# Performance work log

Measured on AMD Instinct MI355X. Metric: run time of the kernel, lower is better.

The kernel has to match this reference:

```python
import jax, jax.numpy as jnp
import numpy as np

B = 256        # graphs per batch
NPG = 256      # nodes per graph (uniform -> to_dense_batch is a reshape, mask = ones)
NTOT = B * NPG
E = 1_048_576
F_IN = 64
HID = 128
HEADS = 5
K1, K2 = 32, 8
MEMH = 100
NCLS = 12
TAU = 1.0
EPS = 1e-8


def setup_inputs() -> dict:
    key = jax.random.key(0)
    ks = jax.random.split(key, 24)
    f32 = jnp.float32
    def nrm(k, shape, s=0.05):
        return jax.random.normal(k, shape, f32) * s
    inp = {
        "x": jax.random.normal(ks[0], (NTOT, F_IN), f32),
        "edge_index": jax.random.randint(ks[1], (2, E), 0, NTOT, jnp.int32),
        "batch": jnp.repeat(jnp.arange(B, dtype=jnp.int32), NPG),
        # GraphConv q0 (num_feats -> hidden): lin_rel (bias) + lin_root (no bias)
        "W_rel0": nrm(ks[2], (F_IN, HID)), "b_rel0": jnp.zeros((HID,), f32),
        "W_root0": nrm(ks[3], (F_IN, HID)),
        # GraphConv q1 (hidden -> hidden)
        "W_rel1": nrm(ks[4], (HID, HID)), "b_rel1": jnp.zeros((HID,), f32),
        "W_root1": nrm(ks[5], (HID, HID)),
        # BatchNorm1d affine params
        "bn_gamma": jnp.ones((HID,), f32), "bn_beta": jnp.zeros((HID,), f32),
        # MemConv layer 0: keys ~ U[0,1) as torch.rand, conv1x1 [heads], lin F->MEMH
        "keys0": jax.random.uniform(ks[6], (HEADS, K1, HID), f32),
        "convw0": nrm(ks[7], (HEADS,), 0.2),
        "lin_W0": nrm(ks[8], (HID, MEMH)), "lin_b0": jnp.zeros((MEMH,), f32),
        # MemConv layer 1 (num_features = mem_hidden_dim)
        "keys1": jax.random.uniform(ks[9], (HEADS, K2, MEMH), f32),
        "convw1": nrm(ks[10], (HEADS,), 0.2),
        "lin_W1": nrm(ks[11], (MEMH, MEMH)), "lin_b1": jnp.zeros((MEMH,), f32),
        # MLP head
        "mlp_W1": nrm(ks[12], (MEMH, 50)), "mlp_b1": jnp.zeros((50,), f32),
        "mlp_W2": nrm(ks[13], (50, NCLS)), "mlp_b2": jnp.zeros((NCLS,), f32),
    }
    return inp


def _graph_conv(x, src, dst, W_rel, b_rel, W_root):
    # PyG GraphConv, aggr='add': out_i = lin_rel(sum_{j in N(i)} x_j) + lin_root(x_i)
    msg = x[src]                                            # [E, F] gather
    aggr = jax.ops.segment_sum(msg, dst, num_segments=NTOT)  # [N, F] scatter-add
    return aggr @ W_rel + b_rel + x @ W_root


def _kl_reg(C):
    P = C ** 2
    cn = C.sum(axis=-2, keepdims=True) + EPS
    P = P / cn
    pn = P.sum(axis=-1, keepdims=True) + EPS
    P = P / pn
    return 100.0 * (P * (jnp.log(P + EPS) - jnp.log(C + EPS))).sum()


def _mem_conv(Q, keys, conv_w, lin_W, lin_b, mask):
    # Q: [B, N, F]; keys: [H, K, F]; mask: [B, N] or None
    # pairwise L2 distance via norm expansion (same math as the broadcast-diff)
    qsq = (Q * Q).sum(-1)                                   # [B, N]
    ksq = (keys * keys).sum(-1)                             # [H, K]
    qk = jnp.einsum('bnf,hkf->bhnk', Q, keys)               # [B, H, N, K]
    d2 = qsq[:, None, :, None] + ksq[None, :, None, :] - 2.0 * qk
    C = jnp.sqrt(jnp.maximum(d2, 1e-12))
    if mask is not None:
        ext = mask[:, None, :, None]                        # [B,1,N,1]
        C = C * ext
    # gmn kernel: student-t style normalization over keys
    C = (1.0 + C * C / TAU) ** (-(0.5 * TAU + 0.5))
    C = C / C.sum(axis=-1, keepdims=True)
    if mask is not None:
        C = C * ext
    # conv1x1 over heads (no bias) then squeeze head dim
    C = jnp.einsum('h,bhnk->bnk', conv_w, C)
    C = jax.nn.softmax(C, axis=-1)                          # [B, N, K]
    if mask is not None:
        C = C * mask[:, :, None]
    kl = _kl_reg(C)
    V = jnp.einsum('bnk,bnf->bkf', C, Q)                    # [B, K, F]
    out = jax.nn.leaky_relu(V @ lin_W + lin_b)              # slope 0.01 (torch default)
    return out, kl


def reference(x, edge_index, batch, W_rel0, b_rel0, W_root0, W_rel1, b_rel1,
              W_root1, bn_gamma, bn_beta, keys0, convw0, lin_W0, lin_b0,
              keys1, convw1, lin_W1, lin_b1, mlp_W1, mlp_b1, mlp_W2, mlp_b2):
    src, dst = edge_index[0], edge_index[1]
    q = jax.nn.relu(_graph_conv(x, src, dst, W_rel0, b_rel0, W_root0))
    q = jax.nn.relu(_graph_conv(q, src, dst, W_rel1, b_rel1, W_root1))
    # BatchNorm1d over all (padded-)node rows, training stats, eps=1e-5
    mu = q.mean(axis=0)
    var = ((q - mu) ** 2).mean(axis=0)
    q = (q - mu) * jax.lax.rsqrt(var + 1e-5) * bn_gamma + bn_beta
    Q = q.reshape(B, NPG, HID)                              # to_dense_batch (uniform graphs)
    mask = jnp.ones((B, NPG), jnp.float32)
    q1, kl1 = _mem_conv(Q, keys0, convw0, lin_W0, lin_b0, mask)
    q2, kl2 = _mem_conv(q1, keys1, convw1, lin_W1, lin_b1, None)
    h = q2.mean(axis=-2)                                    # [B, MEMH]
    yh = jax.nn.leaky_relu(h @ mlp_W1 + mlp_b1) @ mlp_W2 + mlp_b2
    return yh, (kl1 + kl2) / NTOT
```

## Files before the change

### kernel.cpp

```cpp
#include <hip/hip_runtime.h>
#include <hip/hip_bf16.h>

#define NTOT   65536
#define NEDGE  1048576
#define HEADS  5
#define K1     32
#define K2     8
#define MEMH   100
#define EPSF   1e-8f

#define OFF_DEG     0x0000000
#define OFF_CURSOR  0x0040000
#define OFF_WT1     0x0040000
#define OFF_WT2     0x0050000
#define OFF_OFFS    0x0080000
#define OFF_BNSUM   0x00C0000
#define OFF_BNSQ    0x00C0400
#define OFF_SCALE   0x00C0800
#define OFF_SHIFT   0x00C0A00
#define OFF_KSQ0    0x00C0C00
#define OFF_KSQ1    0x00C0E80
#define OFF_KL      0x00C0F40
#define OFF_FLAG    0x00C0F60
#define OFF_W       0x00C1000
#define OFF_K0B     0x0128000
#define OFF_CN      0x0134000
#define OFF_CSR     0x0140000
#define OFF_A       0x0540000
#define OFF_AH128   0x0540000
#define OFF_AL128   0x1540000
#define OFF_AH64    0x0540000
#define OFF_AL64    0x0D40000
#define OFF_B       0x2540000
#define OFF_QH      0x2540000
#define OFF_QL      0x3540000
#define OFF_C       0x4540000
#define OFF_XH      0x4540000
#define OFF_XL      0x4D40000
#define OFF_CG      0x4540000
#define OFF_V       0x4D40000
#define OFF_MQ1     0x5140000
#define OFF_MQ2     0x5460000

#define W_WREL0  0
#define W_BREL0  8192
#define W_WROOT0 8320
#define W_WREL1  16512
#define W_BREL1  32896
#define W_WROOT1 33024
#define W_GAMMA  49408
#define W_BETA   49536
#define W_KEYS0  49664
#define W_CONVW0 70144
#define W_LINW0  70149
#define W_LINB0  82949
#define W_KEYS1  83049
#define W_CONVW1 87049
#define W_LINW1  87054
#define W_LINB1  97054
#define W_MLPW1  97154
#define W_MLPB1  102154
#define W_MLPW2  102204
#define W_MLPB2  102804
#define W_TOTAL  102816

typedef __attribute__((ext_vector_type(8))) short  bf16x8;
typedef __attribute__((ext_vector_type(4))) float  f32x4;

__device__ __forceinline__ float bf2f(unsigned short u){
  union { unsigned int i; float f; } v; v.i = ((unsigned int)u) << 16; return v.f;
}
__device__ __forceinline__ unsigned short f2bf(float f){
  union { float f; unsigned int i; } v; v.f = f;
  unsigned int r = (v.i + 0x7FFFu + ((v.i >> 16) & 1u)) >> 16;
  return (unsigned short)r;
}

__device__ const int g_seg[21] = {0,8192,8320,16512,32896,33024,49408,49536,49664,
                                  70144,70149,82949,83049,87049,87054,97054,97154,
                                  102154,102204,102804,102816};
struct WPtrs { const void* p[20]; };

__global__ void k_detect(const unsigned short* __restrict__ xr, int* flag){
  int t = threadIdx.x & 63;
  unsigned short u = xr[2*t];
  int e = (u >> 7) & 0xFF;
  bool plaus = (u != 0) && (e >= 115) && (e <= 135);
  unsigned long long m = __ballot(plaus);
  if(t == 0) flag[0] = (__popcll(m) >= 48) ? 1 : 0;
}

__global__ __launch_bounds__(256) void k_cvtx(const void* __restrict__ xin,
                                              const int* __restrict__ flag,
                                              unsigned short* __restrict__ xH,
                                              unsigned short* __restrict__ xL){
  int i = blockIdx.x*256 + threadIdx.x;
  float v;
  if(flag[0]) v = bf2f(((const unsigned short*)xin)[i]);
  else        v = ((const float*)xin)[i];
  unsigned short h = f2bf(v);
  xH[i] = h;
  xL[i] = f2bf(v - bf2f(h));
}

__global__ __launch_bounds__(256) void k_cvtw(WPtrs wp, const int* __restrict__ flag,
                                              float* __restrict__ wout){
  int i = blockIdx.x*256 + threadIdx.x;
  if(i >= W_TOTAL) return;
  int s = 0;
  #pragma unroll
  for(int k=0;k<20;k++) if(i >= g_seg[k+1]) s = k+1;
  int j = i - g_seg[s];
  const void* src = wp.p[s];
  wout[i] = flag[0] ? bf2f(((const unsigned short*)src)[j]) : ((const float*)src)[j];
}

__global__ __launch_bounds__(256) void k_cvtaux(const float* __restrict__ W,
                                                unsigned short* __restrict__ k0b,
                                                unsigned short* __restrict__ wt1,
                                                unsigned short* __restrict__ wt2){
  int i = blockIdx.x*256 + threadIdx.x;
  if(i < HEADS*K1*128) k0b[i] = f2bf(W[W_KEYS0 + i]);
  if(i < 128*64){
    int col = i>>6, k = i&63;
    float wr = W[W_WREL0  + k*128 + col];
    float wo = W[W_WROOT0 + k*128 + col];
    unsigned short rh = f2bf(wr), oh = f2bf(wo);
    wt1[i]         = rh;
    wt1[ 8192 + i] = f2bf(wr - bf2f(rh));
    wt1[16384 + i] = oh;
    wt1[24576 + i] = f2bf(wo - bf2f(oh));
  }
  if(i < 128*128){
    int col = i>>7, k = i&127;
    float wr = W[W_WREL1  + k*128 + col];
    float wo = W[W_WROOT1 + k*128 + col];
    unsigned short rh = f2bf(wr), oh = f2bf(wo);
    wt2[i]         = rh;
    wt2[16384 + i] = f2bf(wr - bf2f(rh));
    wt2[32768 + i] = oh;
    wt2[49152 + i] = f2bf(wo - bf2f(oh));
  }
}

__global__ __launch_bounds__(256) void k_init(int* deg, int* cursor,
                                              unsigned long long* bnsum,
                                              unsigned long long* bnsq, float* kl, float* cn){
  int i = blockIdx.x*256 + threadIdx.x;
  if(i < NTOT){ deg[i]=0; cursor[i]=0; }
  if(i < 128){ bnsum[i]=0ULL; bnsq[i]=0ULL; }
  if(i < 2) kl[i]=0.f;
  if(i < 256*32) cn[i]=0.f;
}

__global__ __launch_bounds__(256) void k_count(const int* __restrict__ dst, int* deg){
  int e = blockIdx.x*256 + threadIdx.x;
  atomicAdd(&deg[dst[e]], 1);
}

__global__ __launch_bounds__(1024) void k_scan(const int* __restrict__ deg, int* __restrict__ offs){
  __shared__ int ts[1024];
  const int t = threadIdx.x;
  const int base = t*64;
  int s = 0;
  for(int i=0;i<64;i++) s += deg[base+i];
  ts[t] = s; __syncthreads();
  for(int off=1; off<1024; off<<=1){
    int v = (t>=off) ? ts[t-off] : 0;
    __syncthreads();
    ts[t] += v;
    __syncthreads();
  }
  int run = (t==0) ? 0 : ts[t-1];
  for(int i=0;i<64;i++){ offs[base+i]=run; run += deg[base+i]; }
}

__global__ __launch_bounds__(256) void k_fill(const int* __restrict__ src, const int* __restrict__ dst,
                                              const int* __restrict__ offs, int* cursor,
                                              unsigned short* __restrict__ csr){
  int e = blockIdx.x*256 + threadIdx.x;
  int d = dst[e];
  int p = atomicAdd(&cursor[d], 1);
  csr[offs[d] + p] = (unsigned short)src[e];
}

__global__ __launch_bounds__(256) void k_aggr64(const unsigned short* __restrict__ xH,
                                                const int* __restrict__ offs, const int* __restrict__ deg,
                                                const unsigned short* __restrict__ csr,
                                                unsigned short* __restrict__ aH,
                                                unsigned short* __restrict__ aL){
  const int wid  = (blockIdx.x*256 + threadIdx.x) >> 6;
  const int lane = threadIdx.x & 63;
  const int sub = lane >> 4, fl = lane & 15;
  const int beg = offs[wid], n = deg[wid];
  float4 acc = {0.f,0.f,0.f,0.f};
  int i = 0;
  for(; i+32 <= n; i += 32){
    int s[8];
    #pragma unroll
    for(int j=0;j<8;j++) s[j] = csr[beg + i + 4*j + sub];
    #pragma unroll
    for(int j=0;j<8;j++){
      ushort4 u = *(const ushort4*)(xH + (size_t)s[j]*64 + fl*4);
      acc.x += bf2f(u.x); acc.y += bf2f(u.y); acc.z += bf2f(u.z); acc.w += bf2f(u.w);
    }
  }
  for(; i < n; i += 4){
    if(i + sub < n){
      int s = csr[beg + i + sub];
      ushort4 u = *(const ushort4*)(xH + (size_t)s*64 + fl*4);
      acc.x += bf2f(u.x); acc.y += bf2f(u.y); acc.z += bf2f(u.z); acc.w += bf2f(u.w);
    }
  }
  acc.x += __shfl_xor(acc.x, 16); acc.y += __shfl_xor(acc.y, 16);
  acc.z += __shfl_xor(acc.z, 16); acc.w += __shfl_xor(acc.w, 16);
  acc.x += __shfl_xor(acc.x, 32); acc.y += __shfl_xor(acc.y, 32);
  acc.z += __shfl_xor(acc.z, 32); acc.w += __shfl_xor(acc.w, 32);
  if(sub == 0){
    ushort4 h, l;
    h.x=f2bf(acc.x); l.x=f2bf(acc.x-bf2f(h.x));
    h.y=f2bf(acc.y); l.y=f2bf(acc.y-bf2f(h.y));
    h.z=f2bf(acc.z); l.z=f2bf(acc.z-bf2f(h.z));
    h.w=f2bf(acc.w); l.w=f2bf(acc.w-bf2f(h.w));
    *(ushort4*)(aH + (size_t)wid*64 + fl*4) = h;
    *(ushort4*)(aL + (size_t)wid*64 + fl*4) = l;
  }
}

__global__ __launch_bounds__(256) void k_aggr128(const unsigned short* __restrict__ qH,
                                                 const int* __restrict__ offs, const int* __restrict__ deg,
                                                 const unsigned short* __restrict__ csr,
                                                 unsigned short* __restrict__ aH,
                                                 unsigned short* __restrict__ aL){
  const int wid  = (blockIdx.x*256 + threadIdx.x) >> 6;
  const int lane = threadIdx.x & 63;
  const int sub = lane >> 5, fl = lane & 31;
  const int beg = offs[wid], n = deg[wid];
  float4 acc = {0.f,0.f,0.f,0.f};
  int i = 0;
  for(; i+16 <= n; i += 16){
    int s[8];
    #pragma unroll
    for(int j=0;j<8;j++) s[j] = csr[beg + i + 2*j + sub];
    #pragma unroll
    for(int j=0;j<8;j++){
      ushort4 u = *(const ushort4*)(qH + (size_t)s[j]*128 + fl*4);
      acc.x += bf2f(u.x); acc.y += bf2f(u.y); acc.z += bf2f(u.z); acc.w += bf2f(u.w);
    }
  }
  for(; i < n; i += 2){
    if(i + sub < n){
      int s = csr[beg + i + sub];
      ushort4 u = *(const ushort4*)(qH + (size_t)s*128 + fl*4);
      acc.x += bf2f(u.x); acc.y += bf2f(u.y); acc.z += bf2f(u.z); acc.w += bf2f(u.w);
    }
  }
  acc.x += __shfl_xor(acc.x, 32); acc.y += __shfl_xor(acc.y, 32);
  acc.z += __shfl_xor(acc.z, 32); acc.w += __shfl_xor(acc.w, 32);
  if(sub == 0){
    ushort4 h, l;
    h.x=f2bf(acc.x); l.x=f2bf(acc.x-bf2f(h.x));
    h.y=f2bf(acc.y); l.y=f2bf(acc.y-bf2f(h.y));
    h.z=f2bf(acc.z); l.z=f2bf(acc.z-bf2f(h.z));
    h.w=f2bf(acc.w); l.w=f2bf(acc.w-bf2f(h.w));
    *(ushort4*)(aH + (size_t)wid*128 + fl*4) = h;
    *(ushort4*)(aL + (size_t)wid*128 + fl*4) = l;
  }
}

template<int KD>
__global__ __launch_bounds__(256) void k_ling(const unsigned short* __restrict__ AH,
                                              const unsigned short* __restrict__ AL,
                                              const unsigned short* XH,
                                              const unsigned short* XL,
                                              const unsigned short* __restrict__ WT,
                                              const float* __restrict__ W, int bofs,
                                              unsigned short* outH,
                                              unsigned short* outL){
  constexpr int NK = KD/32;
  const int t = threadIdx.x;
  const int wv = t>>6, lane = t&63, quad = lane>>4, m = lane&15;
  const int rbase = blockIdx.x*128;
  const int c0 = (wv*2)*16 + m;
  const int c1 = (wv*2+1)*16 + m;

  bf16x8 BrH0[NK], BrL0[NK], BoH0[NK], BoL0[NK];
  bf16x8 BrH1[NK], BrL1[NK], BoH1[NK], BoL1[NK];
  #pragma unroll
  for(int ks=0; ks<NK; ks++){
    const size_t o0 = (size_t)c0*KD + ks*32 + quad*8;
    const size_t o1 = (size_t)c1*KD + ks*32 + quad*8;
    BrH0[ks] = *(const bf16x8*)(WT + o0);
    BrL0[ks] = *(const bf16x8*)(WT + 128*KD + o0);
    BoH0[ks] = *(const bf16x8*)(WT + 256*KD + o0);
    BoL0[ks] = *(const bf16x8*)(WT + 384*KD + o0);
    BrH1[ks] = *(const bf16x8*)(WT + o1);
    BrL1[ks] = *(const bf16x8*)(WT + 128*KD + o1);
    BoH1[ks] = *(const bf16x8*)(WT + 256*KD + o1);
    BoL1[ks] = *(const bf16x8*)(WT + 384*KD + o1);
  }
  const float b0 = W[bofs + c0];
  const float b1 = W[bofs + c1];

  for(int rt=0; rt<8; rt++){
    const int r0 = rbase + rt*16;
    bf16x8 fah[NK], fal[NK], fxh[NK], fxl[NK];
    #pragma unroll
    for(int ks=0; ks<NK; ks++){
      const size_t o = (size_t)(r0+m)*KD + ks*32 + quad*8;
      fah[ks] = *(const bf16x8*)(AH + o);
      fal[ks] = *(const bf16x8*)(AL + o);
      fxh[ks] = *(const bf16x8*)(XH + o);
      fxl[ks] = *(const bf16x8*)(XL + o);
    }
    f32x4 a0 = {0.f,0.f,0.f,0.f}, a1 = {0.f,0.f,0.f,0.f};
    #pragma unroll
    for(int ks=0; ks<NK; ks++){
      a0 = __builtin_amdgcn_mfma_f32_16x16x32_bf16(fah[ks], BrH0[ks], a0, 0,0,0);
      a1 = __builtin_amdgcn_mfma_f32_16x16x32_bf16(fah[ks], BrH1[ks], a1, 0,0,0);
      a0 = __builtin_amdgcn_mfma_f32_16x16x32_bf16(fal[ks], BrH0[ks], a0, 0,0,0);
      a1 = __builtin_amdgcn_mfma_f32_16x16x32_bf16(fal[ks], BrH1[ks], a1, 0,0,0);
      a0 = __builtin_amdgcn_mfma_f32_16x16x32_bf16(fah[ks], BrL0[ks], a0, 0,0,0);
      a1 = __builtin_amdgcn_mfma_f32_16x16x32_bf16(fah[ks], BrL1[ks], a1, 0,0,0);
      a0 = __builtin_amdgcn_mfma_f32_16x16x32_bf16(fxh[ks], BoH0[ks], a0, 0,0,0);
      a1 = __builtin_amdgcn_mfma_f32_16x16x32_bf16(fxh[ks], BoH1[ks], a1, 0,0,0);
      a0 = __builtin_amdgcn_mfma_f32_16x16x32_bf16(fxl[ks], BoH0[ks], a0, 0,0,0);
      a1 = __builtin_amdgcn_mfma_f32_16x16x32_bf16(fxl[ks], BoH1[ks], a1, 0,0,0);
      a0 = __builtin_amdgcn_mfma_f32_16x16x32_bf16(fxh[ks], BoL0[ks], a0, 0,0,0);
      a1 = __builtin_amdgcn_mfma_f32_16x16x32_bf16(fxh[ks], BoL1[ks], a1, 0,0,0);
    }
    __syncthreads();
    #pragma unroll
    for(int i=0;i<4;i++){
      const size_t orow = (size_t)(r0 + quad*4 + i)*128;
      float v0 = fmaxf(a0[i] + b0, 0.f);
      unsigned short h0 = f2bf(v0);
      outH[orow + c0] = h0;
      outL[orow + c0] = f2bf(v0 - bf2f(h0));
      float v1 = fmaxf(a1[i] + b1, 0.f);
      unsigned short h1 = f2bf(v1);
      outH[orow + c1] = h1;
      outL[orow + c1] = f2bf(v1 - bf2f(h1));
    }
  }
}

__global__ __launch_bounds__(128) void k_bnstats(const unsigned short* __restrict__ qH,
                                                 const unsigned short* __restrict__ qL,
                                                 double* bnsum, double* bnsq){
  const int j = threadIdx.x;
  const int r0 = blockIdx.x*128;
  float s=0.f, s2=0.f;
  for(int r=0;r<128;r++){
    size_t o = (size_t)(r0+r)*128 + j;
    float v = bf2f(qH[o]) + bf2f(qL[o]);
    s += v; s2 += v*v;
  }
  atomicAdd(&bnsum[j], (double)s);
  atomicAdd(&bnsq[j], (double)s2);
}

__global__ __launch_bounds__(256) void k_bnfin(const double* __restrict__ bnsum, const double* __restrict__ bnsq,
                                               const float* __restrict__ W,
                                               float* scale, float* shift, float* ksq0, float* ksq1){
  const int t = threadIdx.x;
  if(t < 128){
    double mu  = bnsum[t] / (double)NTOT;
    double var = bnsq[t] / (double)NTOT - mu*mu;
    if(var < 0.0) var = 0.0;
    float sc = W[W_GAMMA + t] * rsqrtf((float)var + 1e-5f);
    scale[t] = sc;
    shift[t] = W[W_BETA + t] - (float)mu * sc;
  }
  if(t < HEADS*K1){
    float s=0.f;
    for(int f=0;f<128;f++){ float v = W[W_KEYS0 + t*128 + f]; s += v*v; }
    ksq0[t] = s;
  }
  if(t < HEADS*K2){
    float s=0.f;
    for(int f=0;f<100;f++){ float v = W[W_KEYS1 + t*100 + f]; s += v*v; }
    ksq1[t] = s;
  }
}

__global__ __launch_bounds__(256) void k_memA(
    const unsigned short* __restrict__ qH, const unsigned short* __restrict__ qL,
    const float* __restrict__ scale, const float* __restrict__ shift,
    const unsigned short* __restrict__ k0b,
    const float* __restrict__ W, const float* __restrict__ ksq,
    float* __restrict__ Cg, float* __restrict__ cn)
{
  __shared__ unsigned short Qb[64*136];
  __shared__ float qkL[160*68];
  __shared__ float wsumL[64*36];
  __shared__ float qsqL[64];
  __shared__ float rsL[64*6];
  const int bid = blockIdx.x;
  const int r0 = bid*64;
  const int t = threadIdx.x;
  const int wv = t>>6, lane = t&63, quad = lane>>4, m = lane&15;

  for(int idx=t; idx<64*32; idx+=256){
    int r = idx>>5, c4 = (idx&31)*4;
    size_t o = (size_t)(r0+r)*128 + c4;
    ushort4 uh = *(const ushort4*)(qH + o);
    ushort4 ul = *(const ushort4*)(qL + o);
    float4 s = *(const float4*)(scale + c4);
    float4 h = *(const float4*)(shift + c4);
    ushort4 ob;
    ob.x = f2bf((bf2f(uh.x)+bf2f(ul.x))*s.x + h.x);
    ob.y = f2bf((bf2f(uh.y)+bf2f(ul.y))*s.y + h.y);
    ob.z = f2bf((bf2f(uh.z)+bf2f(ul.z))*s.z + h.z);
    ob.w = f2bf((bf2f(uh.w)+bf2f(ul.w))*s.w + h.w);
    *(ushort4*)(Qb + r*136 + c4) = ob;
  }
  __syncthreads();

  {
    bf16x8 a[4];
    #pragma unroll
    for(int ks=0;ks<4;ks++)
      a[ks] = *(const bf16x8*)(Qb + (wv*16+m)*136 + ks*32 + quad*8);
    for(int nb=0; nb<10; nb++){
      f32x4 acc = {0.f,0.f,0.f,0.f};
      const bf16x8* brow = (const bf16x8*)(k0b + (size_t)(nb*16+m)*128);
      #pragma unroll
      for(int ks=0;ks<4;ks++)
        acc = __builtin_amdgcn_mfma_f32_16x16x32_bf16(a[ks], brow[ks*4+quad], acc,0,0,0);
      *(f32x4*)(qkL + (nb*16+m)*68 + wv*16 + quad*4) = acc;
    }
  }
  if(t < 64){
    float s = 0.f;
    for(int j=0;j<16;j++){
      bf16x8 v = *(const bf16x8*)(Qb + t*136 + j*8);
      #pragma unroll
      for(int e=0;e<8;e++){ float f = bf2f((unsigned short)v[e]); s += f*f; }
    }
    qsqL[t] = s;
  }
  __syncthreads();

  {
    int row = t & 63, g = t >> 6;
    float q2 = qsqL[row];
    #pragma unroll
    for(int pass=0; pass<2; pass++){
      int h = g + pass*4;
      if(h < HEADS){
        float rs = 0.f;
        for(int k=0;k<32;k++){
          float d2 = q2 + ksq[h*32+k] - 2.f*qkL[(h*32+k)*68 + row];
          d2 = fmaxf(d2, 1e-12f);
          rs += 1.f/(1.f+d2);
        }
        rsL[row*6+h] = W[W_CONVW0+h]/fmaxf(rs,1e-20f);
      }
    }
  }
  __syncthreads();

  {
    int row = t & 63, kq = t >> 6;
    float q2 = qsqL[row];
    for(int kk=0; kk<8; kk++){
      int k = kq*8+kk;
      float wsum = 0.f;
      #pragma unroll
      for(int h=0;h<HEADS;h++){
        float d2 = q2 + ksq[h*32+k] - 2.f*qkL[(h*32+k)*68 + row];
        d2 = fmaxf(d2, 1e-12f);
        wsum += rsL[row*6+h]/(1.f+d2);
      }
      wsumL[row*36+k] = wsum;
    }
  }
  __syncthreads();

  if(t < 64){
    float mx = -1e30f;
    #pragma unroll
    for(int k=0;k<32;k++) mx = fmaxf(mx, wsumL[t*36+k]);
    float cv[32]; float se = 0.f;
    #pragma unroll
    for(int k=0;k<32;k++){ float e = __expf(wsumL[t*36+k]-mx); cv[k]=e; se+=e; }
    float inv = 1.f/se;
    #pragma unroll
    for(int k=0;k<32;k++){ cv[k]*=inv; wsumL[t*36+k]=cv[k]; }
    float4* dst = (float4*)(Cg + (size_t)(r0+t)*32);
    #pragma unroll
    for(int k4=0;k4<8;k4++)
      dst[k4] = (float4){cv[k4*4],cv[k4*4+1],cv[k4*4+2],cv[k4*4+3]};
  }
  __syncthreads();
  if(t < 32){
    float s = 0.f;
    for(int r=0;r<64;r++) s += wsumL[r*36+t];
    atomicAdd(&cn[(bid>>2)*32 + t], s);
  }
}

__global__ __launch_bounds__(256) void k_memB(const float* __restrict__ Cg,
                                              const float* __restrict__ cn,
                                              float* __restrict__ klacc){
  __shared__ float cn_s[32];
  __shared__ float red_s[4];
  const int b = blockIdx.x, t = threadIdx.x;
  if(t < 32) cn_s[t] = cn[b*32+t] + EPSF;
  __syncthreads();
  const float* crow = Cg + ((size_t)b*256 + t)*32;
  float cv[32]; float pn = 0.f;
  #pragma unroll
  for(int k4=0;k4<8;k4++){
    float4 u = *(const float4*)(crow + k4*4);
    cv[k4*4]=u.x; cv[k4*4+1]=u.y; cv[k4*4+2]=u.z; cv[k4*4+3]=u.w;
  }
  #pragma unroll
  for(int k=0;k<32;k++) pn += cv[k]*cv[k]/cn_s[k];
  pn += EPSF;
  float acc = 0.f;
  #pragma unroll
  for(int k=0;k<32;k++){
    float P = cv[k]*cv[k]/(cn_s[k]*pn);
    acc += P*(__logf(P+EPSF) - __logf(cv[k]+EPSF));
  }
  #pragma unroll
  for(int off=32; off>0; off>>=1) acc += __shfl_down(acc, off);
  if((t&63)==0) red_s[t>>6] = acc;
  __syncthreads();
  if(t==0) atomicAdd(klacc, 100.f*(red_s[0]+red_s[1]+red_s[2]+red_s[3]));
}

__global__ __launch_bounds__(256) void k_memV(const float* __restrict__ Cg,
                                              const unsigned short* __restrict__ qH,
                                              const unsigned short* __restrict__ qL,
                                              const float* __restrict__ scale,
                                              const float* __restrict__ shift,
                                              float* __restrict__ V){
  __shared__ float Cs[256*36];
  __shared__ float Qs[256*32];
  const int b  = blockIdx.x >> 2;
  const int f0 = (blockIdx.x & 3) * 32;
  const int t = threadIdx.x;
  for(int idx=t; idx<256*8; idx+=256){
    int n = idx>>3, k4 = (idx&7)*4;
    *(float4*)(Cs + n*36 + k4) = *(const float4*)(Cg + ((size_t)b*256+n)*32 + k4);
  }
  for(int idx=t; idx<256*8; idx+=256){
    int n = idx>>3, j4 = (idx&7)*4;
    size_t o = ((size_t)b*256+n)*128 + f0 + j4;
    ushort4 uh = *(const ushort4*)(qH + o);
    ushort4 ul = *(const ushort4*)(qL + o);
    float4 s = *(const float4*)(scale + f0 + j4);
    float4 h = *(const float4*)(shift + f0 + j4);
    *(float4*)(Qs + n*32 + j4) = (float4){
      (bf2f(uh.x)+bf2f(ul.x))*s.x + h.x,
      (bf2f(uh.y)+bf2f(ul.y))*s.y + h.y,
      (bf2f(uh.z)+bf2f(ul.z))*s.z + h.z,
      (bf2f(uh.w)+bf2f(ul.w))*s.w + h.w};
  }
  __syncthreads();
  const int k = t & 31, fg = t >> 5;
  float v0=0.f,v1=0.f,v2=0.f,v3=0.f;
  for(int n=0;n<256;n++){
    float c = Cs[n*36+k];
    float4 q = *(const float4*)(Qs + n*32 + fg*4);
    v0 += c*q.x; v1 += c*q.y; v2 += c*q.z; v3 += c*q.w;
  }
  *(float4*)(V + ((size_t)b*32 + k)*128 + f0 + fg*4) = (float4){v0,v1,v2,v3};
}

__global__ __launch_bounds__(256) void k_memL(const float* __restrict__ V,
                                              const float* __restrict__ W,
                                              float* __restrict__ mq1){
  __shared__ float Vs[32*132];
  const int b = blockIdx.x, t = threadIdx.x;
  for(int idx=t; idx<32*32; idx+=256){
    int k = idx>>5, j4 = (idx&31)*4;
    *(float4*)(Vs + k*132 + j4) = *(const float4*)(V + ((size_t)b*32+k)*128 + j4);
  }
  __syncthreads();
  for(int idx=t; idx<K1*MEMH; idx+=256){
    int k = idx/100, mc = idx - k*100;
    float a = W[W_LINB0 + mc];
    for(int f=0; f<128; f++) a += Vs[k*132+f]*W[W_LINW0 + f*100 + mc];
    mq1[(size_t)(b*32+k)*100 + mc] = (a>0.f) ? a : 0.01f*a;
  }
}

__global__ __launch_bounds__(256) void k_memconv1(
    const float* __restrict__ mq1, const float* __restrict__ W,
    const float* __restrict__ ksq, float* __restrict__ mq2, float* __restrict__ klacc)
{
  __shared__ float Qs[32*104];
  __shared__ float Ks[40*100];
  __shared__ float QKs[32*40];
  __shared__ float Cs[32*8];
  __shared__ float cn_s[8];
  __shared__ float pn_s[32];
  __shared__ float qsq_s[32];
  __shared__ float Vs[8*100];
  __shared__ float red_s[4];
  const int b = blockIdx.x, t = threadIdx.x;

  for(int idx=t; idx<32*100; idx+=256){
    int n = idx/100, f = idx - n*100;
    Qs[n*104+f] = mq1[(size_t)b*3200 + idx];
  }
  for(int idx=t; idx<40*100; idx+=256) Ks[idx] = W[W_KEYS1 + idx];
  __syncthreads();

  if(t < 32){ float s=0.f; for(int f=0;f<100;f++){ float v=Qs[t*104+f]; s+=v*v; } qsq_s[t]=s; }
  for(int idx=t; idx<32*40; idx+=256){
    int n = idx/40, c = idx - n*40;
    float a = 0.f;
    for(int f=0;f<100;f++) a += Qs[n*104+f]*Ks[c*100+f];
    QKs[idx] = a;
  }
  __syncthreads();

  if(t < 32){
    float wsum[8];
    #pragma unroll
    for(int k=0;k<8;k++) wsum[k]=0.f;
    for(int h=0;h<HEADS;h++){
      float cw = W[W_CONVW1 + h];
      float c[8]; float rs=0.f;
      #pragma unroll
      for(int k=0;k<8;k++){
        float d2 = qsq_s[t] + ksq[h*8+k] - 2.f*QKs[t*40 + h*8+k];
        d2 = fmaxf(d2, 1e-12f);
        float cc = 1.f/(1.f+d2);
        c[k]=cc; rs+=cc;
      }
      float sc = cw/fmaxf(rs, 1e-20f);
      #pragma unroll
      for(int k=0;k<8;k++) wsum[k] += c[k]*sc;
    }
    float mx = wsum[0];
    #pragma unroll
    for(int k=1;k<8;k++) mx = fmaxf(mx, wsum[k]);
    float se=0.f;
    #pragma unroll
    for(int k=0;k<8;k++){ float e=__expf(wsum[k]-mx); wsum[k]=e; se+=e; }
    float inv = 1.f/se;
    #pragma unroll
    for(int k=0;k<8;k++) Cs[t*8+k] = wsum[k]*inv;
  }
  __syncthreads();
  if(t < 8){ float s=0.f; for(int n=0;n<32;n++) s += Cs[n*8+t]; cn_s[t]=s+EPSF; }
  __syncthreads();
  if(t < 32){
    float p=0.f;
    #pragma unroll
    for(int k=0;k<8;k++){ float sv=Cs[t*8+k]; p += sv*sv/cn_s[k]; }
    pn_s[t]=p+EPSF;
  }
  __syncthreads();

  float acc;
  {
    int n = t>>3, k = t&7;
    float sv = Cs[t];
    float P = sv*sv/(cn_s[k]*pn_s[n]);
    acc = P*(__logf(P+EPSF) - __logf(sv+EPSF));
  }
  #pragma unroll
  for(int off=32; off>0; off>>=1) acc += __shfl_down(acc, off);
  if((t&63)==0) red_s[t>>6] = acc;

  for(int idx=t; idx<8*100; idx+=256){
    int k = idx/100, f = idx - k*100;
    float a=0.f;
    for(int n=0;n<32;n++) a += Cs[n*8+k]*Qs[n*104+f];
    Vs[idx] = a;
  }
  __syncthreads();

  if(t==0) atomicAdd(klacc, 100.f*(red_s[0]+red_s[1]+red_s[2]+red_s[3]));

  for(int idx=t; idx<8*100; idx+=256){
    int k = idx/100, mc = idx - k*100;
    float a = W[W_LINB1 + mc];
    for(int f=0;f<100;f++) a += Vs[k*100+f]*W[W_LINW1 + f*100 + mc];
    mq2[(size_t)b*800 + idx] = (a>0.f) ? a : 0.01f*a;
  }
}

__global__ __launch_bounds__(128) void k_final(const float* __restrict__ mq2,
                                               const float* __restrict__ W,
                                               const int* __restrict__ flag,
                                               const float* __restrict__ kl,
                                               void* __restrict__ out){
  __shared__ float h_s[100];
  __shared__ float hid_s[50];
  const int b = blockIdx.x, t = threadIdx.x;
  if(t < 100){
    float s=0.f;
    #pragma unroll
    for(int k=0;k<8;k++) s += mq2[(size_t)b*800 + k*100 + t];
    h_s[t] = s*0.125f;
  }
  __syncthreads();
  if(t < 50){
    float a = W[W_MLPB1 + t];
    for(int f=0;f<100;f++) a += h_s[f]*W[W_MLPW1 + f*50 + t];
    hid_s[t] = (a>0.f) ? a : 0.01f*a;
  }
  __syncthreads();
  if(t < 12){
    float a = W[W_MLPB2 + t];
    #pragma unroll
    for(int j=0;j<50;j++) a += hid_s[j]*W[W_MLPW2 + j*12 + t];
    if(flag[0]) ((__hip_bfloat16*)out)[b*12+t] = __float2bfloat16(a);
    else        ((float*)out)[b*12+t] = a;
  }
  if(b==0 && t==64){
    float v = (kl[0]+kl[1]) * (1.f/65536.f);
    if(flag[0]) ((__hip_bfloat16*)out)[3072] = __float2bfloat16(v);
    else        ((float*)out)[3072] = v;
  }
}

extern "C" void kernel_launch(void* const* d_in, const int* in_sizes, int n_in,
                              void* d_out, int out_size, void* d_ws, size_t ws_size,
                              hipStream_t stream) {
  (void)in_sizes; (void)n_in; (void)out_size; (void)ws_size;
  const void* x   = d_in[0];
  const int*  ei  = (const int*)d_in[1];
  const int* src = ei;
  const int* dst = ei + NEDGE;

  WPtrs wp;
  for(int i=0;i<20;i++) wp.p[i] = d_in[3+i];

  char* w = (char*)d_ws;
  int*    deg    = (int*)   (w + OFF_DEG);
  int*    cursor = (int*)   (w + OFF_CURSOR);
  int*    offs   = (int*)   (w + OFF_OFFS);
  double* bnsum  = (double*)(w + OFF_BNSUM);
  double* bnsq   = (double*)(w + OFF_BNSQ);
  float*  scale  = (float*) (w + OFF_SCALE);
  float*  shift  = (float*) (w + OFF_SHIFT);
  float*  ksq0   = (float*) (w + OFF_KSQ0);
  float*  ksq1   = (float*) (w + OFF_KSQ1);
  float*  kl     = (float*) (w + OFF_KL);
  int*    flag   = (int*)   (w + OFF_FLAG);
  float*  Wc     = (float*) (w + OFF_W);
  unsigned short* k0b = (unsigned short*)(w + OFF_K0B);
  unsigned short* wt1 = (unsigned short*)(w + OFF_WT1);
  unsigned short* wt2 = (unsigned short*)(w + OFF_WT2);
  float*  cn     = (float*) (w + OFF_CN);
  unsigned short* csr = (unsigned short*)(w + OFF_CSR);
  unsigned short* agH64  = (unsigned short*)(w + OFF_AH64);
  unsigned short* agL64  = (unsigned short*)(w + OFF_AL64);
  unsigned short* agH128 = (unsigned short*)(w + OFF_AH128);
  unsigned short* agL128 = (unsigned short*)(w + OFF_AL128);
  unsigned short* qvH    = (unsigned short*)(w + OFF_QH);
  unsigned short* qvL    = (unsigned short*)(w + OFF_QL);
  unsigned short* xcH    = (unsigned short*)(w + OFF_XH);
  unsigned short* xcL    = (unsigned short*)(w + OFF_XL);
  float*  Cg     = (float*) (w + OFF_CG);
  float*  Vbuf   = (float*) (w + OFF_V);
  float*  mq1    = (float*) (w + OFF_MQ1);
  float*  mq2    = (float*) (w + OFF_MQ2);

  unsigned short* qbnH = qvH;
  unsigned short* qbnL = qvL;

  k_detect <<<1,      64, 0, stream>>>((const unsigned short*)x, flag);
  k_init   <<<256,   256, 0, stream>>>(deg, cursor, (unsigned long long*)bnsum, (unsigned long long*)bnsq, kl, cn);
  k_count  <<<4096,  256, 0, stream>>>(dst, deg);
  k_scan   <<<1,    1024, 0, stream>>>(deg, offs);
  k_fill   <<<4096,  256, 0, stream>>>(src, dst, offs, cursor, csr);
  k_cvtx   <<<16384, 256, 0, stream>>>(x, flag, xcH, xcL);
  k_cvtw   <<<402,   256, 0, stream>>>(wp, flag, Wc);
  k_cvtaux <<<80,    256, 0, stream>>>(Wc, k0b, wt1, wt2);
  k_aggr64 <<<16384, 256, 0, stream>>>(xcH, offs, deg, csr, agH64, agL64);
  k_ling<64> <<<512, 256, 0, stream>>>(agH64, agL64, xcH, xcL, wt1, Wc, W_BREL0, qvH, qvL);
  k_aggr128<<<16384, 256, 0, stream>>>(qvH, offs, deg, csr, agH128, agL128);
  k_ling<128><<<512, 256, 0, stream>>>(agH128, agL128, qvH, qvL, wt2, Wc, W_BREL1, qbnH, qbnL);
  k_bnstats<<<512,   128, 0, stream>>>(qbnH, qbnL, bnsum, bnsq);
  k_bnfin  <<<1,     256, 0, stream>>>(bnsum, bnsq, Wc, scale, shift, ksq0, ksq1);
  k_memA   <<<1024,  256, 0, stream>>>(qbnH, qbnL, scale, shift, k0b, Wc, ksq0, Cg, cn);
  k_memB   <<<256,   256, 0, stream>>>(Cg, cn, kl);
  k_memV   <<<1024,  256, 0, stream>>>(Cg, qbnH, qbnL, scale, shift, Vbuf);
  k_memL   <<<256,   256, 0, stream>>>(Vbuf, Wc, mq1);
  k_memconv1<<<256,  256, 0, stream>>>(mq1, Wc, ksq1, mq2, kl+1);
  k_final  <<<256,   128, 0, stream>>>(mq2, Wc, flag, kl, d_out);
}
```

Baseline: 567.9 us.

## Build CSR via two-level LDS bucket sort instead of global atomics

Replaces the count / single-block scan / atomic fill CSR construction with a two-pass bucket sort. Edges are first binned by destination high byte using shared-memory histograms and a per-block staged scatter. Each bucket is then sorted locally in LDS to produce the CSR, per-node degrees and offsets. The aim is to remove contended global atomics, the serial 65536-entry scan and scattered 2-byte writes. In exchange, each bucket must hold at most 8192 edges to fit the shared buffers, which holds for uniformly random destinations but not for skewed graphs.

```diff
diff --git a/kernel.cpp b/kernel.cpp
--- a/kernel.cpp
+++ b/kernel.cpp
@@ -25,6 +25,9 @@
 #define OFF_W       0x00C1000
 #define OFF_K0B     0x0128000
 #define OFF_CN      0x0134000
+#define OFF_BH      0x013C000
+#define OFF_EBASE   0x013C400
+#define OFF_BCUR    0x013C800
 #define OFF_CSR     0x0140000
 #define OFF_A       0x0540000
 #define OFF_AH128   0x0540000
@@ -32,6 +35,7 @@
 #define OFF_AH64    0x0540000
 #define OFF_AL64    0x0D40000
 #define OFF_B       0x2540000
+#define OFF_EBUF    0x2540000
 #define OFF_QH      0x2540000
 #define OFF_QL      0x3540000
 #define OFF_C       0x4540000
@@ -143,45 +147,113 @@
   }
 }
 
-__global__ __launch_bounds__(256) void k_init(int* deg, int* cursor,
-                                              unsigned long long* bnsum,
-                                              unsigned long long* bnsq, float* kl, float* cn){
+__global__ __launch_bounds__(256) void k_init(unsigned long long* bnsum,
+                                              unsigned long long* bnsq, float* kl, float* cn,
+                                              int* bhist){
   int i = blockIdx.x*256 + threadIdx.x;
-  if(i < NTOT){ deg[i]=0; cursor[i]=0; }
   if(i < 128){ bnsum[i]=0ULL; bnsq[i]=0ULL; }
   if(i < 2) kl[i]=0.f;
   if(i < 256*32) cn[i]=0.f;
-}
-
-__global__ __launch_bounds__(256) void k_count(const int* __restrict__ dst, int* deg){
-  int e = blockIdx.x*256 + threadIdx.x;
-  atomicAdd(&deg[dst[e]], 1);
-}
-
-__global__ __launch_bounds__(1024) void k_scan(const int* __restrict__ deg, int* __restrict__ offs){
-  __shared__ int ts[1024];
+  if(i < 256) bhist[i]=0;
+}
+
+__global__ __launch_bounds__(256) void k_bin1(const int* __restrict__ dst, int* bhist){
+  __shared__ int hist[256];
   const int t = threadIdx.x;
-  const int base = t*64;
-  int s = 0;
-  for(int i=0;i<64;i++) s += deg[base+i];
-  ts[t] = s; __syncthreads();
-  for(int off=1; off<1024; off<<=1){
+  hist[t] = 0; __syncthreads();
+  const int e0 = blockIdx.x*4096 + t;
+  #pragma unroll 4
+  for(int j=0;j<16;j++) atomicAdd(&hist[dst[e0 + j*256] >> 8], 1);
+  __syncthreads();
+  if(hist[t]) atomicAdd(&bhist[t], hist[t]);
+}
+
+__global__ __launch_bounds__(256) void k_bscan(const int* __restrict__ bhist,
+                                               int* ebase, int* bcur){
+  __shared__ int ts[256];
+  const int t = threadIdx.x;
+  ts[t] = bhist[t]; __syncthreads();
+  for(int off=1; off<256; off<<=1){
     int v = (t>=off) ? ts[t-off] : 0;
-    __syncthreads();
-    ts[t] += v;
-    __syncthreads();
-  }
-  int run = (t==0) ? 0 : ts[t-1];
-  for(int i=0;i<64;i++){ offs[base+i]=run; run += deg[base+i]; }
-}
-
-__global__ __launch_bounds__(256) void k_fill(const int* __restrict__ src, const int* __restrict__ dst,
-                                              const int* __restrict__ offs, int* cursor,
-                                              unsigned short* __restrict__ csr){
-  int e = blockIdx.x*256 + threadIdx.x;
-  int d = dst[e];
-  int p = atomicAdd(&cursor[d], 1);
-  csr[offs[d] + p] = (unsigned short)src[e];
+    __syncthreads(); ts[t] += v; __syncthreads();
+  }
+  int ex = (t==0) ? 0 : ts[t-1];
+  ebase[t] = ex; bcur[t] = ex;
+}
+
+__global__ __launch_bounds__(256) void k_bin2(const int* __restrict__ src, const int* __restrict__ dst,
+                                              int* bcur, unsigned int* __restrict__ ebuf){
+  __shared__ int hist[256], lofs[256], lcur[256], gbase[256];
+  __shared__ unsigned int sbuf[4096];
+  const int t = threadIdx.x;
+  hist[t] = 0; __syncthreads();
+  const int e0 = blockIdx.x*4096;
+  unsigned int pair[16]; int bk[16];
+  #pragma unroll 4
+  for(int j=0;j<16;j++){
+    int e = e0 + t + j*256;
+    int s = src[e], d = dst[e];
+    pair[j] = (((unsigned)d)<<16) | (unsigned)s;
+    bk[j] = d>>8;
+    atomicAdd(&hist[bk[j]], 1);
+  }
+  __syncthreads();
+  lcur[t] = hist[t]; __syncthreads();
+  for(int off=1; off<256; off<<=1){
+    int v = (t>=off) ? lcur[t-off] : 0;
+    __syncthreads(); lcur[t] += v; __syncthreads();
+  }
+  lofs[t] = (t==0) ? 0 : lcur[t-1];
+  __syncthreads();
+  lcur[t] = lofs[t];
+  if(hist[t]) gbase[t] = atomicAdd(&bcur[t], hist[t]);
+  __syncthreads();
+  #pragma unroll 4
+  for(int j=0;j<16;j++){
+    int p = atomicAdd(&lcur[bk[j]], 1);
+    sbuf[p] = pair[j];
+  }
+  __syncthreads();
+  const int n = hist[t], lo = lofs[t], go = gbase[t];
+  for(int i=0;i<n;i++) ebuf[go + i] = sbuf[lo + i];
+}
+
+__global__ __launch_bounds__(256) void k_fine(const unsigned int* __restrict__ ebuf,
+                                              const int* __restrict__ ebase,
+                                              unsigned short* __restrict__ csr,
+                                              int* __restrict__ deg, int* __restrict__ offs){
+  __shared__ int ldeg[256], lofs[256], lcur[256];
+  __shared__ unsigned int led[8192];
+  __shared__ unsigned short lcsr[8192];
+  const int b = blockIdx.x, t = threadIdx.x;
+  const int base = ebase[b];
+  const int n = ((b==255) ? NEDGE : ebase[b+1]) - base;
+  ldeg[t] = 0; __syncthreads();
+  for(int i=t; i<n; i+=256){
+    unsigned int p = ebuf[base+i];
+    led[i] = p;
+    atomicAdd(&ldeg[(p>>16)&255], 1);
+  }
+  __syncthreads();
+  lcur[t] = ldeg[t]; __syncthreads();
+  for(int off=1; off<256; off<<=1){
+    int v = (t>=off) ? lcur[t-off] : 0;
+    __syncthreads(); lcur[t] += v; __syncthreads();
+  }
+  lofs[t] = (t==0) ? 0 : lcur[t-1];
+  __syncthreads();
+  lcur[t] = lofs[t];
+  __syncthreads();
+  for(int i=t; i<n; i+=256){
+    unsigned int p = led[i];
+    int d = (p>>16)&255;
+    int pos = atomicAdd(&lcur[d], 1);
+    lcsr[pos] = (unsigned short)(p & 0xFFFF);
+  }
+  __syncthreads();
+  for(int i=t; i<n; i+=256) csr[base+i] = lcsr[i];
+  deg[b*256 + t]  = ldeg[t];
+  offs[b*256 + t] = base + lofs[t];
 }
 
 __global__ __launch_bounds__(256) void k_aggr64(const unsigned short* __restrict__ xH,
@@ -737,7 +809,6 @@
 
   char* w = (char*)d_ws;
   int*    deg    = (int*)   (w + OFF_DEG);
-  int*    cursor = (int*)   (w + OFF_CURSOR);
   int*    offs   = (int*)   (w + OFF_OFFS);
   double* bnsum  = (double*)(w + OFF_BNSUM);
   double* bnsq   = (double*)(w + OFF_BNSQ);
@@ -752,7 +823,11 @@
   unsigned short* wt1 = (unsigned short*)(w + OFF_WT1);
   unsigned short* wt2 = (unsigned short*)(w + OFF_WT2);
   float*  cn     = (float*) (w + OFF_CN);
+  int*    bhist  = (int*)   (w + OFF_BH);
+  int*    ebase  = (int*)   (w + OFF_EBASE);
+  int*    bcur   = (int*)   (w + OFF_BCUR);
   unsigned short* csr = (unsigned short*)(w + OFF_CSR);
+  unsigned int*   ebuf = (unsigned int*)(w + OFF_EBUF);
   unsigned short* agH64  = (unsigned short*)(w + OFF_AH64);
   unsigned short* agL64  = (unsigned short*)(w + OFF_AL64);
   unsigned short* agH128 = (unsigned short*)(w + OFF_AH128);
@@ -770,10 +845,11 @@
   unsigned short* qbnL = qvL;
 
   k_detect <<<1,      64, 0, stream>>>((const unsigned short*)x, flag);
-  k_init   <<<256,   256, 0, stream>>>(deg, cursor, (unsigned long long*)bnsum, (unsigned long long*)bnsq, kl, cn);
-  k_count  <<<4096,  256, 0, stream>>>(dst, deg);
-  k_scan   <<<1,    1024, 0, stream>>>(deg, offs);
-  k_fill   <<<4096,  256, 0, stream>>>(src, dst, offs, cursor, csr);
+  k_init   <<<32,    256, 0, stream>>>((unsigned long long*)bnsum, (unsigned long long*)bnsq, kl, cn, bhist);
+  k_bin1   <<<256,   256, 0, stream>>>(dst, bhist);
+  k_bscan  <<<1,     256, 0, stream>>>(bhist, ebase, bcur);
+  k_bin2   <<<256,   256, 0, stream>>>(src, dst, bcur, ebuf);
+  k_fine   <<<256,   256, 0, stream>>>(ebuf, ebase, csr, deg, offs);
   k_cvtx   <<<16384, 256, 0, stream>>>(x, flag, xcH, xcL);
   k_cvtw   <<<402,   256, 0, stream>>>(wp, flag, Wc);
   k_cvtaux <<<80,    256, 0, stream>>>(Wc, k0b, wt1, wt2);
```

After: 479.1 us. 1.19x faster.
